# Optimization experiments

Measured on AMD Instinct MI355X. Metric: run time of the kernel, lower is better.

The kernel has to match this reference:

```python
import jax, jax.numpy as jnp
import numpy as np

B, C, H, W = 4, 256, 64, 64
C8 = C // 8


def setup_inputs() -> dict:
    key = jax.random.key(0)
    ks = jax.random.split(key, 8)
    x = jax.random.normal(ks[0], (B, C, H, W), dtype=jnp.float32)
    valid = jax.random.uniform(ks[1], (B, 1, H, W), dtype=jnp.float32)
    # 1x1 conv weights (kernel_size=1 -> plain channel matmul) + biases
    Wq = jax.random.normal(ks[2], (C8, C), dtype=jnp.float32) * 0.05
    bq = jnp.zeros((C8,), dtype=jnp.float32)
    Wk = jax.random.normal(ks[3], (C8, C), dtype=jnp.float32) * 0.05
    bk = jnp.zeros((C8,), dtype=jnp.float32)
    Wv = jax.random.normal(ks[4], (C, C), dtype=jnp.float32) * 0.05
    bv = jnp.zeros((C,), dtype=jnp.float32)
    gamma = jnp.asarray(0.5, dtype=jnp.float32)  # nonzero so attention path matters
    return {"x": x, "valid": valid, "Wq": Wq, "bq": bq, "Wk": Wk, "bk": bk,
            "Wv": Wv, "bv": bv, "gamma": gamma}


def reference(x, valid, Wq, bq, Wk, bk, Wv, bv, gamma):
    b, c, h, w = x.shape
    n = h * w
    xf = x.reshape(b, c, n)                                   # [B,C,N]
    # valid is already at (H,W): nearest interpolate to same size is identity
    v = valid.reshape(b, 1, n)                                # [B,1,N]
    q = jnp.einsum('oc,bcn->bno', Wq, xf) + bq                # [B,N,C//8]
    k = jnp.einsum('oc,bcn->bon', Wk, xf) + bk[None, :, None] # [B,C//8,N]
    energy = jnp.einsum('bno,bom->bnm', q, k)                 # [B,N,N]
    attn = jax.nn.softmax(energy, axis=-1)
    va = attn * v                                             # mask columns
    scale = 1.0 / jnp.sum(va, axis=2, keepdims=True)          # per-row renorm
    sa = va * scale                                           # [B,N,N]
    pv = jnp.einsum('oc,bcn->bon', Wv, xf) + bv[None, :, None]  # [B,C,N]
    out = jnp.einsum('bon,bmn->bom', pv, sa)                  # bmm(V, A^T)
    out = out.reshape(b, c, h, w)
    return gamma * out + x, sa
```

## Files before the change

kernel.cpp:

```cpp
#include <hip/hip_runtime.h>

typedef unsigned short u16;
typedef unsigned int u32;
typedef __attribute__((ext_vector_type(8))) short short8;
typedef __attribute__((ext_vector_type(4))) float f32x4;
typedef __attribute__((ext_vector_type(2))) unsigned int u32x2;
typedef __attribute__((ext_vector_type(4))) unsigned int u32x4;

#define BB 4
#define CC 256
#define NT 4096
#define L2E 1.4426950408889634f

__device__ __forceinline__ float b2f(u16 v) {
    union { u32 u; float f; } c; c.u = ((u32)v) << 16; return c.f;
}
__device__ __forceinline__ u16 f2b(float f) {
    union { float f; u32 u; } c; c.f = f;
    u32 u = c.u;
    return (u16)((u + 0x7fffu + ((u >> 16) & 1u)) >> 16);
}

__global__ __launch_bounds__(256) void kproj(
    const float* __restrict__ x,
    const float* __restrict__ Wq, const float* __restrict__ bq,
    const float* __restrict__ Wk, const float* __restrict__ bk,
    const float* __restrict__ Wv, const float* __restrict__ bv,
    u16* __restrict__ qh, u16* __restrict__ ql,
    u16* __restrict__ kh, u16* __restrict__ kl,
    u16* __restrict__ pvw)
{
    __shared__ __align__(16) float lA[32][68];
    __shared__ __align__(16) float lX[32][68];
    const int mt = blockIdx.x, nt = blockIdx.y, b = blockIdx.z;
    const int t = threadIdx.x;
    const int tx = t & 15, ty = t >> 4;
    const int n0 = nt * 64;

    float acc[4][4];
    #pragma unroll
    for (int i = 0; i < 4; ++i)
        #pragma unroll
        for (int j = 0; j < 4; ++j) acc[i][j] = 0.f;

    const int rA = t >> 2, kqA = (t & 3) * 8;
    const int rgA = mt * 64 + rA;
    const float* wrow;
    if (rgA < 32)      wrow = Wq + rgA * 256;
    else if (rgA < 64) wrow = Wk + (rgA - 32) * 256;
    else               wrow = Wv + (rgA - 64) * 256;
    const int kX = t >> 3, nn8 = (t & 7) * 8;
    const float* xrow = x + ((size_t)(b * CC + kX)) * NT + n0 + nn8;

    for (int k0 = 0; k0 < 256; k0 += 32) {
        f32x4 wa = *(const f32x4*)(wrow + k0 + kqA);
        f32x4 wb = *(const f32x4*)(wrow + k0 + kqA + 4);
        f32x4 xa = *(const f32x4*)(xrow + (size_t)k0 * NT);
        f32x4 xb = *(const f32x4*)(xrow + (size_t)k0 * NT + 4);
        __syncthreads();
        #pragma unroll
        for (int j = 0; j < 4; ++j) {
            lA[kqA + j    ][rA] = wa[j];
            lA[kqA + j + 4][rA] = wb[j];
        }
        *(f32x4*)&lX[kX][nn8]     = xa;
        *(f32x4*)&lX[kX][nn8 + 4] = xb;
        __syncthreads();
        #pragma unroll
        for (int k = 0; k < 32; ++k) {
            f32x4 av  = *(const f32x4*)&lA[k][ty * 4];
            f32x4 xvv = *(const f32x4*)&lX[k][tx * 4];
            #pragma unroll
            for (int i = 0; i < 4; ++i)
                #pragma unroll
                for (int j = 0; j < 4; ++j)
                    acc[i][j] = fmaf(av[i], xvv[j], acc[i][j]);
        }
    }

    #pragma unroll
    for (int i = 0; i < 4; ++i) {
        const int rg = mt * 64 + ty * 4 + i;
        float bias;
        if (rg < 32)      bias = bq[rg];
        else if (rg < 64) bias = bk[rg - 32];
        else              bias = bv[rg - 64];
        #pragma unroll
        for (int j = 0; j < 4; ++j) {
            const int n = n0 + tx * 4 + j;
            const float val = acc[i][j] + bias;
            const u16 h = f2b(val);
            const u16 l = f2b(val - b2f(h));
            if (rg < 32) {
                const size_t idx = ((size_t)(b * NT + n)) * 32 + rg;
                qh[idx] = h; ql[idx] = l;
            } else if (rg < 64) {
                const size_t idx = ((size_t)(b * NT + n)) * 32 + (rg - 32);
                kh[idx] = h; kl[idx] = l;
            } else {
                pvw[((size_t)b * CC + (rg - 64)) * NT + n] = f2b(val);
            }
        }
    }
}

#define MFMA_BF16(A, B, C) __builtin_amdgcn_mfma_f32_16x16x32_bf16(A, B, C, 0, 0, 0)

__global__ __launch_bounds__(512, 4) void ksaout(
    const u16* __restrict__ qh, const u16* __restrict__ ql,
    const u16* __restrict__ kh, const u16* __restrict__ kl,
    const float* __restrict__ valid, const u16* __restrict__ pvw,
    const float* __restrict__ x, const float* __restrict__ gamma,
    float* __restrict__ sa, float* __restrict__ outp)
{
    __shared__ __align__(16) u16 lB[3][32][128];
    __shared__ float sred[2][4][16];
    const int b    = blockIdx.y;
    const int m0   = blockIdx.x * 32;
    const int t    = threadIdx.x;
    const int lane = t & 63;
    const int wv   = t >> 6;
    const int quad = lane >> 4, l16 = lane & 15;
    const int rg   = wv >> 2, cq = wv & 3;
    const int swz  = (l16 & 7) << 4;

    const size_t qbase = ((size_t)(b * NT + m0 + rg * 16 + l16)) * 32 + quad * 8;
    const short8 aqh = *(const short8*)(qh + qbase);
    const short8 aql = *(const short8*)(ql + qbase);
    const size_t kbase = (size_t)b * NT * 32 + (size_t)l16 * 32 + quad * 8;
    const float* vbase = valid + (size_t)b * NT;
    const f32x4 zero = {0.f, 0.f, 0.f, 0.f};

    float sacc = 0.f;
    {
        short8 nbh = *(const short8*)(kh + kbase + (size_t)(cq * 64) * 512);
        short8 nbl = *(const short8*)(kl + kbase + (size_t)(cq * 64) * 512);
        f32x4  nv4 = *(const f32x4*)(vbase + (cq * 64) * 16 + quad * 4);
        for (int s = 0; s < 64; ++s) {
            short8 bh = nbh, bl = nbl;
            f32x4 v4 = nv4;
            if (s + 1 < 64) {
                const int ct = cq * 64 + s + 1;
                nbh = *(const short8*)(kh + kbase + (size_t)ct * 512);
                nbl = *(const short8*)(kl + kbase + (size_t)ct * 512);
                nv4 = *(const f32x4*)(vbase + ct * 16 + quad * 4);
            }
            f32x4 d = MFMA_BF16(bh, aqh, zero);
            d = MFMA_BF16(bh, aql, d);
            d = MFMA_BF16(bl, aqh, d);
            #pragma unroll
            for (int i = 0; i < 4; ++i)
                sacc += v4[i] * exp2f(fminf(d[i], 60.f) * L2E);
        }
    }
    sacc += __shfl_xor(sacc, 16, 64);
    sacc += __shfl_xor(sacc, 32, 64);
    if (lane < 16) sred[rg][cq][l16] = sacc;
    __syncthreads();
    const float inv = 1.0f / (sred[rg][0][l16] + sred[rg][1][l16] +
                              sred[rg][2][l16] + sred[rg][3][l16]);

    const u16* pva = pvw + ((size_t)(b * CC + wv * 32 + l16)) * NT + quad * 8;
    float* sap = sa + ((size_t)(b * NT + m0 + rg * 16 + l16)) * NT;
    char* lbB = (char*)&lB[0][0][0];
    const int lwoff = (rg * 16 + l16) * 256 + ((cq * 32 + quad * 8) ^ swz);

    f32x4 acc00 = {0,0,0,0}, acc01 = {0,0,0,0}, acc10 = {0,0,0,0}, acc11 = {0,0,0,0};

#define LOADQK(S, BH, BL, VV)                                                  \
    { int ct_ = (S) * 4 + cq; if (ct_ > 255) ct_ = 255;                        \
      BH = *(const short8*)(kh + kbase + (size_t)ct_ * 512);                   \
      BL = *(const short8*)(kl + kbase + (size_t)ct_ * 512);                   \
      VV = *(const f32x4*)(vbase + ct_ * 16 + quad * 4); }

#define ASTEP(S, J, BUF, BH, BL, VV)                                           \
    { f32x4 d = MFMA_BF16(BH, aqh, zero);                                      \
      d = MFMA_BF16(BH, aql, d);                                               \
      d = MFMA_BF16(BL, aqh, d);                                               \
      f32x4 val;                                                               \
      _Pragma("unroll")                                                        \
      for (int i = 0; i < 4; ++i)                                              \
          val[i] = VV[i] * exp2f(fminf(d[i], 60.f) * L2E) * inv;               \
      *(f32x4*)(sap + (size_t)(S) * 64 + cq * 16 + quad * 4) = val;            \
      u32x2 pk;                                                                \
      pk[0] = (u32)f2b(val[0]) | ((u32)f2b(val[1]) << 16);                     \
      pk[1] = (u32)f2b(val[2]) | ((u32)f2b(val[3]) << 16);                     \
      *(u32x2*)(lbB + (BUF) * 8192 + lwoff + (J) * 128) = pk; }

    short8 qbh0, qbl0, qbh1, qbl1;
    f32x4 qv0, qv1;
    short8 pac[8];

    LOADQK(0, qbh0, qbl0, qv0);
    LOADQK(1, qbh1, qbl1, qv1);
    ASTEP(0, 0, 0, qbh0, qbl0, qv0);
    ASTEP(1, 1, 0, qbh1, qbl1, qv1);
    LOADQK(2, qbh0, qbl0, qv0);
    LOADQK(3, qbh1, qbl1, qv1);
    #pragma unroll
    for (int k4 = 0; k4 < 4; ++k4) {
        pac[k4]     = *(const short8*)(pva + k4 * 32);
        pac[4 + k4] = *(const short8*)(pva + (size_t)16 * NT + k4 * 32);
    }
    asm volatile("s_waitcnt lgkmcnt(0)" ::: "memory");
    __builtin_amdgcn_sched_barrier(0);
    __builtin_amdgcn_s_barrier();
    __builtin_amdgcn_sched_barrier(0);

    for (int p = 0; p < 32; ++p) {
        const int rbuf = p % 3;
        if (p < 31) {
            const int wbuf = (p + 1) % 3;
            ASTEP(2 * p + 2, 0, wbuf, qbh0, qbl0, qv0);
            ASTEP(2 * p + 3, 1, wbuf, qbh1, qbl1, qv1);
            if (p < 30) {
                LOADQK(2 * p + 4, qbh0, qbl0, qv0);
                LOADQK(2 * p + 5, qbh1, qbl1, qv1);
            }
            asm volatile("s_waitcnt lgkmcnt(0)" ::: "memory");
            __builtin_amdgcn_sched_barrier(0);
            __builtin_amdgcn_s_barrier();
            __builtin_amdgcn_sched_barrier(0);
        }
        __builtin_amdgcn_s_setprio(1);
        #pragma unroll
        for (int k4 = 0; k4 < 4; ++k4) {
            const int kby = ((k4 * 64 + quad * 16) ^ swz);
            short8 b0 = *(const short8*)(lbB + rbuf * 8192 + l16 * 256 + kby);
            short8 b1 = *(const short8*)(lbB + rbuf * 8192 + (16 + l16) * 256 + kby);
            acc00 = MFMA_BF16(pac[k4], b0, acc00);
            acc01 = MFMA_BF16(pac[k4], b1, acc01);
            acc10 = MFMA_BF16(pac[4 + k4], b0, acc10);
            acc11 = MFMA_BF16(pac[4 + k4], b1, acc11);
        }
        __builtin_amdgcn_s_setprio(0);
        if (p < 31) {
            #pragma unroll
            for (int k4 = 0; k4 < 4; ++k4) {
                pac[k4]     = *(const short8*)(pva + (size_t)(p + 1) * 128 + k4 * 32);
                pac[4 + k4] = *(const short8*)(pva + (size_t)(p + 1) * 128
                                               + (size_t)16 * NT + k4 * 32);
            }
        }
    }
#undef LOADQK
#undef ASTEP

    const float g = gamma[0];
    #pragma unroll
    for (int ai = 0; ai < 2; ++ai) {
        #pragma unroll
        for (int bi = 0; bi < 2; ++bi) {
            f32x4 acc = (ai == 0) ? ((bi == 0) ? acc00 : acc01)
                                  : ((bi == 0) ? acc10 : acc11);
            #pragma unroll
            for (int i = 0; i < 4; ++i) {
                const int c = wv * 32 + ai * 16 + quad * 4 + i;
                const int m = m0 + bi * 16 + l16;
                const size_t idx = ((size_t)(b * CC + c)) * NT + m;
                outp[idx] = g * acc[i] + x[idx];
            }
        }
    }
}

extern "C" void kernel_launch(void* const* d_in, const int* in_sizes, int n_in,
                              void* d_out, int out_size, void* d_ws, size_t ws_size,
                              hipStream_t stream)
{
    const float* x     = (const float*)d_in[0];
    const float* valid = (const float*)d_in[1];
    const float* Wq    = (const float*)d_in[2];
    const float* bq    = (const float*)d_in[3];
    const float* Wk    = (const float*)d_in[4];
    const float* bk    = (const float*)d_in[5];
    const float* Wv    = (const float*)d_in[6];
    const float* bv    = (const float*)d_in[7];
    const float* gamma = (const float*)d_in[8];

    float* outp = (float*)d_out;
    float* sa   = outp + (size_t)BB * CC * NT;

    u16* qh  = (u16*)d_ws;
    u16* ql  = qh + (size_t)BB * NT * 32;
    u16* kh  = ql + (size_t)BB * NT * 32;
    u16* kl  = kh + (size_t)BB * NT * 32;
    u16* pvw = kl + (size_t)BB * NT * 32;

    kproj<<<dim3(5, 64, BB), 256, 0, stream>>>(x, Wq, bq, Wk, bk, Wv, bv,
                                               qh, ql, kh, kl, pvw);
    ksaout<<<dim3(128, BB), 512, 0, stream>>>(qh, ql, kh, kl, valid, pvw,
                                              x, gamma, sa, outp);
}
```

Baseline: 522.8 us.

## Shrink attention block to 16 query rows with 4 waves and padded LDS

Restructures the fused attention kernel so each block handles 16 query rows with 256 threads instead of 32 rows with 512, doubling the grid. Each wave now owns 64 output channels and streams its pv operands in a double-buffered register rotation interleaved with the MFMAs. The LDS tile is padded instead of XOR-swizzled, and the row-sum pass interleaves key tiles across waves. The intent is better occupancy and latency hiding. The cost is that each block re-reads K and pv, which doubles their global traffic.

```diff
diff --git a/kernel.cpp b/kernel.cpp
--- a/kernel.cpp
+++ b/kernel.cpp
@@ -105,26 +105,26 @@
 }
 
 #define MFMA_BF16(A, B, C) __builtin_amdgcn_mfma_f32_16x16x32_bf16(A, B, C, 0, 0, 0)
-
-__global__ __launch_bounds__(512, 4) void ksaout(
+#define RS   288
+#define LBUF 4608
+
+__global__ __launch_bounds__(256, 4) void ksaout(
     const u16* __restrict__ qh, const u16* __restrict__ ql,
     const u16* __restrict__ kh, const u16* __restrict__ kl,
     const float* __restrict__ valid, const u16* __restrict__ pvw,
     const float* __restrict__ x, const float* __restrict__ gamma,
     float* __restrict__ sa, float* __restrict__ outp)
 {
-    __shared__ __align__(16) u16 lB[3][32][128];
-    __shared__ float sred[2][4][16];
+    __shared__ __align__(16) u16 lP[3 * 16 * 144];
+    __shared__ float sred[4][16];
     const int b    = blockIdx.y;
-    const int m0   = blockIdx.x * 32;
+    const int m0   = blockIdx.x * 16;
     const int t    = threadIdx.x;
     const int lane = t & 63;
-    const int wv   = t >> 6;
+    const int cq   = t >> 6;
     const int quad = lane >> 4, l16 = lane & 15;
-    const int rg   = wv >> 2, cq = wv & 3;
-    const int swz  = (l16 & 7) << 4;
-
-    const size_t qbase = ((size_t)(b * NT + m0 + rg * 16 + l16)) * 32 + quad * 8;
+
+    const size_t qbase = ((size_t)(b * NT + m0 + l16)) * 32 + quad * 8;
     const short8 aqh = *(const short8*)(qh + qbase);
     const short8 aql = *(const short8*)(ql + qbase);
     const size_t kbase = (size_t)b * NT * 32 + (size_t)l16 * 32 + quad * 8;
@@ -133,14 +133,14 @@
 
     float sacc = 0.f;
     {
-        short8 nbh = *(const short8*)(kh + kbase + (size_t)(cq * 64) * 512);
-        short8 nbl = *(const short8*)(kl + kbase + (size_t)(cq * 64) * 512);
-        f32x4  nv4 = *(const f32x4*)(vbase + (cq * 64) * 16 + quad * 4);
+        short8 nbh = *(const short8*)(kh + kbase + (size_t)cq * 512);
+        short8 nbl = *(const short8*)(kl + kbase + (size_t)cq * 512);
+        f32x4  nv4 = *(const f32x4*)(vbase + cq * 16 + quad * 4);
         for (int s = 0; s < 64; ++s) {
             short8 bh = nbh, bl = nbl;
             f32x4 v4 = nv4;
             if (s + 1 < 64) {
-                const int ct = cq * 64 + s + 1;
+                const int ct = (s + 1) * 4 + cq;
                 nbh = *(const short8*)(kh + kbase + (size_t)ct * 512);
                 nbl = *(const short8*)(kl + kbase + (size_t)ct * 512);
                 nv4 = *(const f32x4*)(vbase + ct * 16 + quad * 4);
@@ -155,25 +155,28 @@
     }
     sacc += __shfl_xor(sacc, 16, 64);
     sacc += __shfl_xor(sacc, 32, 64);
-    if (lane < 16) sred[rg][cq][l16] = sacc;
+    if (lane < 16) sred[cq][l16] = sacc;
     __syncthreads();
-    const float inv = 1.0f / (sred[rg][0][l16] + sred[rg][1][l16] +
-                              sred[rg][2][l16] + sred[rg][3][l16]);
-
-    const u16* pva = pvw + ((size_t)(b * CC + wv * 32 + l16)) * NT + quad * 8;
-    float* sap = sa + ((size_t)(b * NT + m0 + rg * 16 + l16)) * NT;
-    char* lbB = (char*)&lB[0][0][0];
-    const int lwoff = (rg * 16 + l16) * 256 + ((cq * 32 + quad * 8) ^ swz);
-
-    f32x4 acc00 = {0,0,0,0}, acc01 = {0,0,0,0}, acc10 = {0,0,0,0}, acc11 = {0,0,0,0};
+    const float inv = 1.0f / (sred[0][l16] + sred[1][l16] +
+                              sred[2][l16] + sred[3][l16]);
+
+    float* sap = sa + ((size_t)(b * NT + m0 + l16)) * NT;
+    char* lpB = (char*)&lP[0];
+    const int lwoff = l16 * RS + cq * 32 + quad * 8;
+    const u16* pva0 = pvw + ((size_t)(b * CC + cq * 64 + l16)) * NT + quad * 8;
+    const u16* pva1 = pva0 + (size_t)16 * NT;
+    const u16* pva2 = pva0 + (size_t)32 * NT;
+    const u16* pva3 = pva0 + (size_t)48 * NT;
+
+    f32x4 acc0 = {0,0,0,0}, acc1 = {0,0,0,0}, acc2 = {0,0,0,0}, acc3 = {0,0,0,0};
 
 #define LOADQK(S, BH, BL, VV)                                                  \
-    { int ct_ = (S) * 4 + cq; if (ct_ > 255) ct_ = 255;                        \
+    { const int ct_ = (S) * 4 + cq;                                            \
       BH = *(const short8*)(kh + kbase + (size_t)ct_ * 512);                   \
       BL = *(const short8*)(kl + kbase + (size_t)ct_ * 512);                   \
       VV = *(const f32x4*)(vbase + ct_ * 16 + quad * 4); }
 
-#define ASTEP(S, J, BUF, BH, BL, VV)                                           \
+#define ASTEP(S, BUF, BH, BL, VV)                                              \
     { f32x4 d = MFMA_BF16(BH, aqh, zero);                                      \
       d = MFMA_BF16(BH, aql, d);                                               \
       d = MFMA_BF16(BL, aqh, d);                                               \
@@ -185,23 +188,32 @@
       u32x2 pk;                                                                \
       pk[0] = (u32)f2b(val[0]) | ((u32)f2b(val[1]) << 16);                     \
       pk[1] = (u32)f2b(val[2]) | ((u32)f2b(val[3]) << 16);                     \
-      *(u32x2*)(lbB + (BUF) * 8192 + lwoff + (J) * 128) = pk; }
-
-    short8 qbh0, qbl0, qbh1, qbl1;
-    f32x4 qv0, qv1;
-    short8 pac[8];
-
-    LOADQK(0, qbh0, qbl0, qv0);
-    LOADQK(1, qbh1, qbl1, qv1);
-    ASTEP(0, 0, 0, qbh0, qbl0, qv0);
-    ASTEP(1, 1, 0, qbh1, qbl1, qv1);
-    LOADQK(2, qbh0, qbl0, qv0);
-    LOADQK(3, qbh1, qbl1, qv1);
-    #pragma unroll
-    for (int k4 = 0; k4 < 4; ++k4) {
-        pac[k4]     = *(const short8*)(pva + k4 * 32);
-        pac[4 + k4] = *(const short8*)(pva + (size_t)16 * NT + k4 * 32);
-    }
+      *(u32x2*)(lpB + (BUF) * LBUF + lwoff + ((S) & 1) * 128) = pk; }
+
+#define LOADPA(G0, G1, G2, G3, OFF)                                            \
+    { G0 = *(const short8*)(pva0 + (OFF));                                     \
+      G1 = *(const short8*)(pva1 + (OFF));                                     \
+      G2 = *(const short8*)(pva2 + (OFF));                                     \
+      G3 = *(const short8*)(pva3 + (OFF)); }
+
+#define PVSLOT(BT, G0, G1, G2, G3)                                             \
+    { acc0 = MFMA_BF16(G0, BT, acc0);                                          \
+      acc1 = MFMA_BF16(G1, BT, acc1);                                          \
+      acc2 = MFMA_BF16(G2, BT, acc2);                                          \
+      acc3 = MFMA_BF16(G3, BT, acc3); }
+
+    short8 kbh0, kbl0, kbh1, kbl1;
+    f32x4 kv0, kv1;
+    short8 pA0, pA1, pA2, pA3, pB0, pB1, pB2, pB3;
+
+    LOADQK(0, kbh0, kbl0, kv0);
+    LOADQK(1, kbh1, kbl1, kv1);
+    ASTEP(0, 0, kbh0, kbl0, kv0);
+    ASTEP(1, 0, kbh1, kbl1, kv1);
+    LOADQK(2, kbh0, kbl0, kv0);
+    LOADQK(3, kbh1, kbl1, kv1);
+    LOADPA(pA0, pA1, pA2, pA3, 0);
+    LOADPA(pB0, pB1, pB2, pB3, 32);
     asm volatile("s_waitcnt lgkmcnt(0)" ::: "memory");
     __builtin_amdgcn_sched_barrier(0);
     __builtin_amdgcn_s_barrier();
@@ -211,55 +223,49 @@
         const int rbuf = p % 3;
         if (p < 31) {
             const int wbuf = (p + 1) % 3;
-            ASTEP(2 * p + 2, 0, wbuf, qbh0, qbl0, qv0);
-            ASTEP(2 * p + 3, 1, wbuf, qbh1, qbl1, qv1);
+            ASTEP(2 * p + 2, wbuf, kbh0, kbl0, kv0);
+            ASTEP(2 * p + 3, wbuf, kbh1, kbl1, kv1);
             if (p < 30) {
-                LOADQK(2 * p + 4, qbh0, qbl0, qv0);
-                LOADQK(2 * p + 5, qbh1, qbl1, qv1);
+                LOADQK(2 * p + 4, kbh0, kbl0, kv0);
+                LOADQK(2 * p + 5, kbh1, kbl1, kv1);
             }
             asm volatile("s_waitcnt lgkmcnt(0)" ::: "memory");
             __builtin_amdgcn_sched_barrier(0);
             __builtin_amdgcn_s_barrier();
             __builtin_amdgcn_sched_barrier(0);
         }
+        const char* lb = lpB + rbuf * LBUF + l16 * RS + quad * 16;
+        short8 bt0 = *(const short8*)(lb);
+        short8 bt1 = *(const short8*)(lb + 64);
+        short8 bt2 = *(const short8*)(lb + 128);
+        short8 bt3 = *(const short8*)(lb + 192);
+        const size_t koff = (size_t)p * 128;
         __builtin_amdgcn_s_setprio(1);
-        #pragma unroll
-        for (int k4 = 0; k4 < 4; ++k4) {
-            const int kby = ((k4 * 64 + quad * 16) ^ swz);
-            short8 b0 = *(const short8*)(lbB + rbuf * 8192 + l16 * 256 + kby);
-            short8 b1 = *(const short8*)(lbB + rbuf * 8192 + (16 + l16) * 256 + kby);
-            acc00 = MFMA_BF16(pac[k4], b0, acc00);
-            acc01 = MFMA_BF16(pac[k4], b1, acc01);
-            acc10 = MFMA_BF16(pac[4 + k4], b0, acc10);
-            acc11 = MFMA_BF16(pac[4 + k4], b1, acc11);
-        }
+        PVSLOT(bt0, pA0, pA1, pA2, pA3);
+        LOADPA(pA0, pA1, pA2, pA3, koff + 64);
+        PVSLOT(bt1, pB0, pB1, pB2, pB3);
+        LOADPA(pB0, pB1, pB2, pB3, koff + 96);
+        PVSLOT(bt2, pA0, pA1, pA2, pA3);
+        if (p < 31) LOADPA(pA0, pA1, pA2, pA3, koff + 128);
+        PVSLOT(bt3, pB0, pB1, pB2, pB3);
+        if (p < 31) LOADPA(pB0, pB1, pB2, pB3, koff + 160);
         __builtin_amdgcn_s_setprio(0);
-        if (p < 31) {
-            #pragma unroll
-            for (int k4 = 0; k4 < 4; ++k4) {
-                pac[k4]     = *(const short8*)(pva + (size_t)(p + 1) * 128 + k4 * 32);
-                pac[4 + k4] = *(const short8*)(pva + (size_t)(p + 1) * 128
-                                               + (size_t)16 * NT + k4 * 32);
-            }
-        }
     }
 #undef LOADQK
 #undef ASTEP
+#undef LOADPA
+#undef PVSLOT
 
     const float g = gamma[0];
+    const int m = m0 + l16;
     #pragma unroll
-    for (int ai = 0; ai < 2; ++ai) {
-        #pragma unroll
-        for (int bi = 0; bi < 2; ++bi) {
-            f32x4 acc = (ai == 0) ? ((bi == 0) ? acc00 : acc01)
-                                  : ((bi == 0) ? acc10 : acc11);
-            #pragma unroll
-            for (int i = 0; i < 4; ++i) {
-                const int c = wv * 32 + ai * 16 + quad * 4 + i;
-                const int m = m0 + bi * 16 + l16;
-                const size_t idx = ((size_t)(b * CC + c)) * NT + m;
-                outp[idx] = g * acc[i] + x[idx];
-            }
+    for (int j = 0; j < 4; ++j) {
+        f32x4 acc = (j == 0) ? acc0 : (j == 1) ? acc1 : (j == 2) ? acc2 : acc3;
+        #pragma unroll
+        for (int i = 0; i < 4; ++i) {
+            const int c = cq * 64 + j * 16 + quad * 4 + i;
+            const size_t idx = ((size_t)(b * CC + c)) * NT + m;
+            outp[idx] = g * acc[i] + x[idx];
         }
     }
 }
@@ -289,6 +295,6 @@
 
     kproj<<<dim3(5, 64, BB), 256, 0, stream>>>(x, Wq, bq, Wk, bk, Wv, bv,
                                                qh, ql, kh, kl, pvw);
-    ksaout<<<dim3(128, BB), 512, 0, stream>>>(qh, ql, kh, kl, valid, pvw,
+    ksaout<<<dim3(256, BB), 256, 0, stream>>>(qh, ql, kh, kl, valid, pvw,
                                               x, gamma, sa, outp);
 }
```

Result: slower. 626.9 us (+19.9%).
